# Kernel tuning notes

Measured on AMD Instinct MI355X. Metric: run time of the kernel, lower is better.

## Reference

```python
import jax, jax.numpy as jnp
import numpy as np

N_USERS = 100000
N_ITEMS = 50000
DIM = 64
NNZ = 10000000
N_LAYERS = 3
N_NODES = N_USERS + N_ITEMS


def setup_inputs() -> dict:
    key = jax.random.key(0)
    k1, k2, k3, k4, k5 = jax.random.split(key, 5)
    # xavier-ish init for embedding tables
    user_emb = jax.random.normal(k1, (N_USERS, DIM), dtype=jnp.float32) * 0.1
    item_emb = jax.random.normal(k2, (N_ITEMS, DIM), dtype=jnp.float32) * 0.1
    # COO representation of the symmetric normalized adjacency
    adj_row = jax.random.randint(k3, (NNZ,), 0, N_NODES, dtype=jnp.int32)
    adj_col = jax.random.randint(k4, (NNZ,), 0, N_NODES, dtype=jnp.int32)
    # normalized values are small positive numbers (d_i^-1/2 * d_j^-1/2)
    adj_val = jax.random.uniform(k5, (NNZ,), dtype=jnp.float32) * 0.01
    return {
        "user_emb": user_emb,
        "item_emb": item_emb,
        "adj_val": adj_val,
        "adj_row": adj_row,
        "adj_col": adj_col,
    }


def reference(user_emb, item_emb, adj_val, adj_row, adj_col):
    # all_emb: [N_NODES, DIM]
    all_emb = jnp.concatenate([user_emb, item_emb], axis=0)
    acc = all_emb  # running sum over layers (incl. layer 0)
    emb = all_emb
    for _ in range(N_LAYERS):
        # SpMM: out[r] += val * emb[c] for each edge (r, c)
        msgs = adj_val[:, None] * emb[adj_col]  # [NNZ, DIM]
        emb = jax.ops.segment_sum(msgs, adj_row, num_segments=N_NODES)
        acc = acc + emb
    mean_emb = acc / jnp.float32(N_LAYERS + 1)
    return mean_emb[:N_USERS], mean_emb[N_USERS:]
```

## Files before the change

### kernel.cpp

```cpp
#include <hip/hip_runtime.h>

#define N_USERS 100000
#define N_ITEMS 50000
#define N_NODES (N_USERS + N_ITEMS)
#define DIM 64
#define NNZ_TOTAL 10000000
#define TOTAL (N_NODES * DIM)
#define TOTAL4 (TOTAL / 4)
#define USZ4 (N_USERS * DIM / 4)

#define BROWS 256
#define NB ((N_NODES + BROWS - 1) / BROWS)
#define SCHUNK 8192
#define SGRD ((NNZ_TOTAL + SCHUNK - 1) / SCHUNK)
#define COLMASK 0x3FFFFu

#define CTSH 14
#define NT 10
#define NKEY (BROWS * NT)

__device__ __forceinline__ float bf2f(unsigned short u) {
    return __uint_as_float(((unsigned)u) << 16);
}
__device__ __forceinline__ unsigned short f2bf(float f) {
    unsigned b = __float_as_uint(f);
    b += 0x7FFFu + ((b >> 16) & 1u);
    return (unsigned short)(b >> 16);
}

__global__ __launch_bounds__(256) void k_init(const float4* __restrict__ user,
                                              const float4* __restrict__ item,
                                              ushort4* __restrict__ T0,
                                              float4* __restrict__ acc) {
    const int stride = gridDim.x * blockDim.x;
    for (int i = blockIdx.x * blockDim.x + threadIdx.x; i < TOTAL4; i += stride) {
        float4 v = (i < USZ4) ? user[i] : item[i - USZ4];
        acc[i] = v;
        ushort4 t;
        t.x = f2bf(v.x); t.y = f2bf(v.y); t.z = f2bf(v.z); t.w = f2bf(v.w);
        T0[i] = t;
    }
}

__global__ __launch_bounds__(256) void k_lhist(const int* __restrict__ row,
                                               int* __restrict__ cnt) {
    __shared__ int h[NB];
    for (int i = threadIdx.x; i < NB; i += 256) h[i] = 0;
    __syncthreads();
    const int g = blockIdx.x;
    const int lo = g * SCHUNK;
    const int hi = (lo + SCHUNK < NNZ_TOTAL) ? lo + SCHUNK : NNZ_TOTAL;
    for (int e = lo + threadIdx.x; e < hi; e += 256)
        atomicAdd(&h[row[e] >> 8], 1);
    __syncthreads();
    for (int b = threadIdx.x; b < NB; b += 256)
        cnt[b * SGRD + g] = h[b];
}

__global__ __launch_bounds__(256) void k_rowsum(const int* __restrict__ cnt,
                                                int* __restrict__ rowsum) {
    __shared__ int lds[256];
    const int b = blockIdx.x;
    const int t = threadIdx.x;
    int s = 0;
    for (int k = t; k < SGRD; k += 256) s += cnt[b * SGRD + k];
    lds[t] = s;
    __syncthreads();
    #pragma unroll
    for (int off = 128; off > 0; off >>= 1) {
        if (t < off) lds[t] += lds[t + off];
        __syncthreads();
    }
    if (t == 0) rowsum[b] = lds[0];
}

__global__ __launch_bounds__(1024) void k_sscan(const int* __restrict__ rowsum,
                                                int* __restrict__ bbase) {
    __shared__ int lds[1024];
    const int t = threadIdx.x;
    const int x = (t < NB) ? rowsum[t] : 0;
    lds[t] = x;
    __syncthreads();
    for (int off = 1; off < 1024; off <<= 1) {
        const int y = (t >= off) ? lds[t - off] : 0;
        __syncthreads();
        lds[t] += y;
        __syncthreads();
    }
    if (t < NB) bbase[t] = lds[t] - x;
    if (t == 1023) bbase[NB] = lds[1023];
}

__global__ __launch_bounds__(1024) void k_rowscan(int* __restrict__ cnt,
                                                  const int* __restrict__ bbase) {
    __shared__ int lds[1024];
    const int b = blockIdx.x;
    const int t = threadIdx.x;
    const int i0 = 2 * t, i1 = 2 * t + 1;
    const int a0 = (i0 < SGRD) ? cnt[b * SGRD + i0] : 0;
    const int a1 = (i1 < SGRD) ? cnt[b * SGRD + i1] : 0;
    const int s = a0 + a1;
    lds[t] = s;
    __syncthreads();
    for (int off = 1; off < 1024; off <<= 1) {
        const int y = (t >= off) ? lds[t - off] : 0;
        __syncthreads();
        lds[t] += y;
        __syncthreads();
    }
    const int pre = bbase[b] + lds[t] - s;
    if (i0 < SGRD) cnt[b * SGRD + i0] = pre;
    if (i1 < SGRD) cnt[b * SGRD + i1] = pre + a0;
}

__global__ __launch_bounds__(1024) void k_lscatter(const int* __restrict__ row,
                                                   const int* __restrict__ col,
                                                   const float* __restrict__ val,
                                                   const int* __restrict__ cnt,
                                                   const int* __restrict__ bbase,
                                                   uint2* __restrict__ tmp) {
    __shared__ uint2 stage[SCHUNK];
    __shared__ int lstartp[1024];
    __shared__ int gbase[NB];
    __shared__ int cur[NB];
    __shared__ int scratch[1024];

    const int g = blockIdx.x;
    const int t = threadIdx.x;
    const int lo = g * SCHUNK;
    const int hi = (lo + SCHUNK < NNZ_TOTAL) ? lo + SCHUNK : NNZ_TOTAL;
    const int n = hi - lo;

    int lcnt = 0;
    if (t < NB) {
        const int base = cnt[t * SGRD + g];
        gbase[t] = base;
        const int nxt = (g == SGRD - 1) ? bbase[t + 1] : cnt[t * SGRD + g + 1];
        lcnt = nxt - base;
    }
    scratch[t] = lcnt;
    __syncthreads();

    for (int off = 1; off < 1024; off <<= 1) {
        const int y = (t >= off) ? scratch[t - off] : 0;
        __syncthreads();
        scratch[t] += y;
        __syncthreads();
    }
    const int ls = (t < NB) ? scratch[t] - lcnt : n;
    lstartp[t] = ls;
    if (t < NB) cur[t] = ls;
    __syncthreads();

    for (int e = lo + t; e < hi; e += 1024) {
        const int r = row[e];
        const unsigned meta = ((unsigned)(r & (BROWS - 1)) << 18) | (unsigned)col[e];
        const int p = atomicAdd(&cur[r >> 8], 1);
        stage[p] = make_uint2(meta, __float_as_uint(val[e]));
    }
    __syncthreads();

    for (int l = t; l < n; l += 1024) {
        int blo = 0, bhi = 1024;
        #pragma unroll
        for (int s = 0; s < 10; ++s) {
            const int mid = (blo + bhi) >> 1;
            if (lstartp[mid] <= l) blo = mid; else bhi = mid;
        }
        tmp[gbase[blo] + (l - lstartp[blo])] = stage[l];
    }
}

__global__ __launch_bounds__(256) void k_bsort(const uint2* __restrict__ tmp,
                                               uint2* __restrict__ csr,
                                               const int* __restrict__ bbase,
                                               int* __restrict__ row_offs) {
    __shared__ int cnt[NKEY];
    __shared__ int curl[NKEY];
    __shared__ int part[256];
    const int tid = threadIdx.x;
    const int b = blockIdx.x;
    const int s = bbase[b];
    const int e = bbase[b + 1];

    for (int k = tid; k < NKEY; k += 256) cnt[k] = 0;
    __syncthreads();
    for (int j = s + tid; j < e; j += 256) {
        const unsigned m = tmp[j].x;
        const int key = (int)(m >> 18) * NT + (int)((m & COLMASK) >> CTSH);
        atomicAdd(&cnt[key], 1);
    }
    __syncthreads();
    const int lo = tid * NT;
    int ssum = 0;
    #pragma unroll
    for (int k = 0; k < NT; ++k) ssum += cnt[lo + k];
    part[tid] = ssum;
    __syncthreads();
    for (int off = 1; off < 256; off <<= 1) {
        const int y = (tid >= off) ? part[tid - off] : 0;
        __syncthreads();
        part[tid] += y;
        __syncthreads();
    }
    int base = part[tid] - ssum;
    #pragma unroll
    for (int k = 0; k < NT; ++k) {
        const int c = cnt[lo + k];
        cnt[lo + k] = base;
        curl[lo + k] = base;
        base += c;
    }
    __syncthreads();
    {
        const int gr = b * BROWS + tid;
        if (gr < N_NODES) row_offs[gr] = s + cnt[tid * NT];
    }
    for (int j = s + tid; j < e; j += 256) {
        const uint2 u = tmp[j];
        const unsigned m = u.x;
        const int key = (int)(m >> 18) * NT + (int)((m & COLMASK) >> CTSH);
        const int p = atomicAdd(&curl[key], 1);
        csr[s + p] = u;
    }
    if (b == 0 && tid == 0) row_offs[N_NODES] = NNZ_TOTAL;
}

template <bool FINAL>
__global__ __launch_bounds__(256) void k_spmm_bf16(const ushort4* __restrict__ T4,
                                                   ushort4* __restrict__ U4,
                                                   float4* __restrict__ ACC4,
                                                   const int* __restrict__ offs,
                                                   const uint2* __restrict__ csr) {
    const int lane = threadIdx.x & 63;
    const int sub  = lane >> 4;
    const int d4   = lane & 15;
    const int r = blockIdx.x * 4 + (threadIdx.x >> 6);
    const int s = offs[r];
    const int e = offs[r + 1];
    float4 acc = make_float4(0.f, 0.f, 0.f, 0.f);
    int j = s + sub;
    for (; j + 12 < e; j += 16) {
        const uint2 e0 = csr[j];
        const uint2 e1 = csr[j + 4];
        const uint2 e2 = csr[j + 8];
        const uint2 e3 = csr[j + 12];
        const ushort4 g0 = T4[(size_t)(e0.x & COLMASK) * 16 + d4];
        const ushort4 g1 = T4[(size_t)(e1.x & COLMASK) * 16 + d4];
        const ushort4 g2 = T4[(size_t)(e2.x & COLMASK) * 16 + d4];
        const ushort4 g3 = T4[(size_t)(e3.x & COLMASK) * 16 + d4];
        const float v0 = __uint_as_float(e0.y);
        const float v1 = __uint_as_float(e1.y);
        const float v2 = __uint_as_float(e2.y);
        const float v3 = __uint_as_float(e3.y);
        acc.x += v0 * bf2f(g0.x) + v1 * bf2f(g1.x) + v2 * bf2f(g2.x) + v3 * bf2f(g3.x);
        acc.y += v0 * bf2f(g0.y) + v1 * bf2f(g1.y) + v2 * bf2f(g2.y) + v3 * bf2f(g3.y);
        acc.z += v0 * bf2f(g0.z) + v1 * bf2f(g1.z) + v2 * bf2f(g2.z) + v3 * bf2f(g3.z);
        acc.w += v0 * bf2f(g0.w) + v1 * bf2f(g1.w) + v2 * bf2f(g2.w) + v3 * bf2f(g3.w);
    }
    for (; j + 4 < e; j += 8) {
        const uint2 e0 = csr[j];
        const uint2 e1 = csr[j + 4];
        const ushort4 g0 = T4[(size_t)(e0.x & COLMASK) * 16 + d4];
        const ushort4 g1 = T4[(size_t)(e1.x & COLMASK) * 16 + d4];
        const float v0 = __uint_as_float(e0.y);
        const float v1 = __uint_as_float(e1.y);
        acc.x += v0 * bf2f(g0.x) + v1 * bf2f(g1.x);
        acc.y += v0 * bf2f(g0.y) + v1 * bf2f(g1.y);
        acc.z += v0 * bf2f(g0.z) + v1 * bf2f(g1.z);
        acc.w += v0 * bf2f(g0.w) + v1 * bf2f(g1.w);
    }
    if (j < e) {
        const uint2 e0 = csr[j];
        const ushort4 g0 = T4[(size_t)(e0.x & COLMASK) * 16 + d4];
        const float v0 = __uint_as_float(e0.y);
        acc.x += v0 * bf2f(g0.x);
        acc.y += v0 * bf2f(g0.y);
        acc.z += v0 * bf2f(g0.z);
        acc.w += v0 * bf2f(g0.w);
    }
    #pragma unroll
    for (int m = 16; m <= 32; m <<= 1) {
        acc.x += __shfl_xor(acc.x, m, 64);
        acc.y += __shfl_xor(acc.y, m, 64);
        acc.z += __shfl_xor(acc.z, m, 64);
        acc.w += __shfl_xor(acc.w, m, 64);
    }
    if (sub == 0) {
        const size_t idx = (size_t)r * 16 + d4;
        float4 a = ACC4[idx];
        if (FINAL) {
            a.x = (a.x + acc.x) * 0.25f;
            a.y = (a.y + acc.y) * 0.25f;
            a.z = (a.z + acc.z) * 0.25f;
            a.w = (a.w + acc.w) * 0.25f;
            ACC4[idx] = a;
        } else {
            ushort4 t;
            t.x = f2bf(acc.x); t.y = f2bf(acc.y); t.z = f2bf(acc.z); t.w = f2bf(acc.w);
            U4[idx] = t;
            a.x += acc.x;
            a.y += acc.y;
            a.z += acc.z;
            a.w += acc.w;
            ACC4[idx] = a;
        }
    }
}

__global__ __launch_bounds__(256) void k_init_f32(const float4* __restrict__ user,
                                                  const float4* __restrict__ item,
                                                  float4* __restrict__ A,
                                                  float4* __restrict__ acc) {
    const int stride = gridDim.x * blockDim.x;
    for (int i = blockIdx.x * blockDim.x + threadIdx.x; i < TOTAL4; i += stride) {
        float4 v = (i < USZ4) ? user[i] : item[i - USZ4];
        A[i] = v;
        acc[i] = v;
    }
}

__global__ __launch_bounds__(256) void k_spmm_atomic(const float* __restrict__ A,
                                                     float* __restrict__ B,
                                                     const float* __restrict__ val,
                                                     const int* __restrict__ row,
                                                     const int* __restrict__ col) {
    const int lane = threadIdx.x & 63;
    int wave = blockIdx.x * (blockDim.x >> 6) + (threadIdx.x >> 6);
    const int nw = gridDim.x * (blockDim.x >> 6);
    for (int e = wave; e < NNZ_TOTAL; e += nw) {
        const float x = A[col[e] * DIM + lane];
        unsafeAtomicAdd(&B[row[e] * DIM + lane], val[e] * x);
    }
}

__global__ __launch_bounds__(256) void k_accadd(float4* __restrict__ acc,
                                                const float4* __restrict__ B) {
    const int stride = gridDim.x * blockDim.x;
    for (int i = blockIdx.x * blockDim.x + threadIdx.x; i < TOTAL4; i += stride) {
        float4 a = acc[i];
        const float4 b = B[i];
        a.x += b.x; a.y += b.y; a.z += b.z; a.w += b.w;
        acc[i] = a;
    }
}

__global__ __launch_bounds__(256) void k_final(float4* __restrict__ acc,
                                               const float4* __restrict__ B) {
    const int stride = gridDim.x * blockDim.x;
    for (int i = blockIdx.x * blockDim.x + threadIdx.x; i < TOTAL4; i += stride) {
        float4 a = acc[i];
        const float4 b = B[i];
        a.x = (a.x + b.x) * 0.25f;
        a.y = (a.y + b.y) * 0.25f;
        a.z = (a.z + b.z) * 0.25f;
        a.w = (a.w + b.w) * 0.25f;
        acc[i] = a;
    }
}

extern "C" void kernel_launch(void* const* d_in, const int* in_sizes, int n_in,
                              void* d_out, int out_size, void* d_ws, size_t ws_size,
                              hipStream_t stream) {
    const float* user = (const float*)d_in[0];
    const float* item = (const float*)d_in[1];
    const float* val  = (const float*)d_in[2];
    const int*   row  = (const int*)d_in[3];
    const int*   col  = (const int*)d_in[4];

    float* acc = (float*)d_out;
    const int eltBlocks = 2048;

    const size_t CSR_BYTES = (size_t)NNZ_TOTAL * 8;
    uint2* csr  = (uint2*)d_ws;
    int*   cnt  = (int*)d_ws;
    char*  reg1 = (char*)d_ws + CSR_BYTES;
    uint2* tmp  = (uint2*)reg1;
    ushort4* T0 = (ushort4*)reg1;
    ushort4* T1 = T0 + TOTAL4;
    int* row_offs = (int*)(reg1 + CSR_BYTES);
    int* bbase    = row_offs + N_NODES + 1;
    int* rowsum   = bbase + NB + 1;

    const size_t needed =
        2 * CSR_BYTES + (size_t)(N_NODES + 1 + 2 * NB + 2) * 4;

    if (ws_size >= needed) {
        k_lhist<<<SGRD, 256, 0, stream>>>(row, cnt);
        k_rowsum<<<NB, 256, 0, stream>>>(cnt, rowsum);
        k_sscan<<<1, 1024, 0, stream>>>(rowsum, bbase);
        k_rowscan<<<NB, 1024, 0, stream>>>(cnt, bbase);
        k_lscatter<<<SGRD, 1024, 0, stream>>>(row, col, val, cnt, bbase, tmp);
        k_bsort<<<NB, 256, 0, stream>>>(tmp, csr, bbase, row_offs);

        k_init<<<eltBlocks, 256, 0, stream>>>((const float4*)user, (const float4*)item,
                                              T0, (float4*)acc);

        const int rowBlocks = N_NODES / 4;
        k_spmm_bf16<false><<<rowBlocks, 256, 0, stream>>>(
            T0, T1, (float4*)acc, row_offs, csr);
        k_spmm_bf16<false><<<rowBlocks, 256, 0, stream>>>(
            T1, T0, (float4*)acc, row_offs, csr);
        k_spmm_bf16<true><<<rowBlocks, 256, 0, stream>>>(
            T0, T1, (float4*)acc, row_offs, csr);
        return;
    }

    float* A2 = (float*)d_ws;
    float* B2 = A2 + TOTAL;
    k_init_f32<<<eltBlocks, 256, 0, stream>>>((const float4*)user, (const float4*)item,
                                              (float4*)A2, (float4*)acc);
    float* Af = A2;
    float* Bf = B2;
    for (int layer = 0; layer < 3; ++layer) {
        hipMemsetAsync(Bf, 0, (size_t)TOTAL * sizeof(float), stream);
        k_spmm_atomic<<<2048, 256, 0, stream>>>(Af, Bf, val, row, col);
        if (layer < 2) {
            k_accadd<<<eltBlocks, 256, 0, stream>>>((float4*)acc, (const float4*)Bf);
            float* t = Af; Af = Bf; Bf = t;
        } else {
            k_final<<<eltBlocks, 256, 0, stream>>>((float4*)acc, (const float4*)Bf);
        }
    }
}
```

Measured before the change: 787.8 us.

## Tile SpMM gathers by column range with LDS row accumulators

The per-bucket sort now orders edges by column tile first, then by row. A new kernel builds per-(tile,row) offset tables. The SpMM kernel assigns 74 rows to each block and walks the 10 column tiles in sequence, accumulating partial row sums in shared memory, so that gathers from the bf16 embedding table stay within a roughly 2 MB column window that can stay cache-resident. In exchange it adds a preprocessing kernel, a block barrier after every tile, and very short per-(row,tile) segments. The old 4-way unrolled gather loop becomes a single-gather loop, which lowers memory-level parallelism.

```diff
diff --git a/kernel.cpp b/kernel.cpp
--- a/kernel.cpp
+++ b/kernel.cpp
@@ -18,6 +18,10 @@
 #define CTSH 14
 #define NT 10
 #define NKEY (BROWS * NT)
+
+#define ROWS_PB 74
+#define RPW 19
+#define SPMM_GRID ((N_NODES + ROWS_PB - 1) / ROWS_PB)
 
 __device__ __forceinline__ float bf2f(unsigned short u) {
     return __uint_as_float(((unsigned)u) << 16);
@@ -173,8 +177,7 @@
 
 __global__ __launch_bounds__(256) void k_bsort(const uint2* __restrict__ tmp,
                                                uint2* __restrict__ csr,
-                                               const int* __restrict__ bbase,
-                                               int* __restrict__ row_offs) {
+                                               const int* __restrict__ bbase) {
     __shared__ int cnt[NKEY];
     __shared__ int curl[NKEY];
     __shared__ int part[256];
@@ -187,7 +190,7 @@
     __syncthreads();
     for (int j = s + tid; j < e; j += 256) {
         const unsigned m = tmp[j].x;
-        const int key = (int)(m >> 18) * NT + (int)((m & COLMASK) >> CTSH);
+        const int key = (int)((m & COLMASK) >> CTSH) * BROWS + (int)(m >> 18);
         atomicAdd(&cnt[key], 1);
     }
     __syncthreads();
@@ -207,103 +210,131 @@
     #pragma unroll
     for (int k = 0; k < NT; ++k) {
         const int c = cnt[lo + k];
-        cnt[lo + k] = base;
         curl[lo + k] = base;
         base += c;
     }
     __syncthreads();
-    {
-        const int gr = b * BROWS + tid;
-        if (gr < N_NODES) row_offs[gr] = s + cnt[tid * NT];
-    }
     for (int j = s + tid; j < e; j += 256) {
         const uint2 u = tmp[j];
         const unsigned m = u.x;
-        const int key = (int)(m >> 18) * NT + (int)((m & COLMASK) >> CTSH);
+        const int key = (int)((m & COLMASK) >> CTSH) * BROWS + (int)(m >> 18);
         const int p = atomicAdd(&curl[key], 1);
         csr[s + p] = u;
     }
-    if (b == 0 && tid == 0) row_offs[N_NODES] = NNZ_TOTAL;
+}
+
+__global__ __launch_bounds__(256) void k_rtoffs(const uint2* __restrict__ csr,
+                                                const int* __restrict__ bbase,
+                                                int* __restrict__ rt_abs) {
+    __shared__ int cnt[NKEY];
+    __shared__ int part[256];
+    const int tid = threadIdx.x;
+    const int b = blockIdx.x;
+    const int s = bbase[b];
+    const int e = bbase[b + 1];
+    for (int k = tid; k < NKEY; k += 256) cnt[k] = 0;
+    __syncthreads();
+    for (int j = s + tid; j < e; j += 256) {
+        const unsigned m = csr[j].x;
+        const int key = (int)((m & COLMASK) >> CTSH) * BROWS + (int)(m >> 18);
+        atomicAdd(&cnt[key], 1);
+    }
+    __syncthreads();
+    const int lo = tid * NT;
+    int ssum = 0;
+    #pragma unroll
+    for (int k = 0; k < NT; ++k) ssum += cnt[lo + k];
+    part[tid] = ssum;
+    __syncthreads();
+    for (int off = 1; off < 256; off <<= 1) {
+        const int y = (tid >= off) ? part[tid - off] : 0;
+        __syncthreads();
+        part[tid] += y;
+        __syncthreads();
+    }
+    int base = part[tid] - ssum;
+    #pragma unroll
+    for (int k = 0; k < NT; ++k) {
+        rt_abs[(size_t)b * NKEY + lo + k] = s + base;
+        base += cnt[lo + k];
+    }
+    if (b == 0 && tid == 0) rt_abs[(size_t)NB * NKEY] = NNZ_TOTAL;
 }
 
 template <bool FINAL>
-__global__ __launch_bounds__(256) void k_spmm_bf16(const ushort4* __restrict__ T4,
-                                                   ushort4* __restrict__ U4,
-                                                   float4* __restrict__ ACC4,
-                                                   const int* __restrict__ offs,
-                                                   const uint2* __restrict__ csr) {
-    const int lane = threadIdx.x & 63;
+__global__ __launch_bounds__(256, 8) void k_spmm_tile(const ushort4* __restrict__ T4,
+                                                      ushort4* __restrict__ U4,
+                                                      float4* __restrict__ ACC4,
+                                                      const int* __restrict__ rt_abs,
+                                                      const uint2* __restrict__ csr) {
+    __shared__ float4 accL[ROWS_PB * 16];
+    const int tid  = threadIdx.x;
+    const int lane = tid & 63;
     const int sub  = lane >> 4;
     const int d4   = lane & 15;
-    const int r = blockIdx.x * 4 + (threadIdx.x >> 6);
-    const int s = offs[r];
-    const int e = offs[r + 1];
-    float4 acc = make_float4(0.f, 0.f, 0.f, 0.f);
-    int j = s + sub;
-    for (; j + 12 < e; j += 16) {
-        const uint2 e0 = csr[j];
-        const uint2 e1 = csr[j + 4];
-        const uint2 e2 = csr[j + 8];
-        const uint2 e3 = csr[j + 12];
-        const ushort4 g0 = T4[(size_t)(e0.x & COLMASK) * 16 + d4];
-        const ushort4 g1 = T4[(size_t)(e1.x & COLMASK) * 16 + d4];
-        const ushort4 g2 = T4[(size_t)(e2.x & COLMASK) * 16 + d4];
-        const ushort4 g3 = T4[(size_t)(e3.x & COLMASK) * 16 + d4];
-        const float v0 = __uint_as_float(e0.y);
-        const float v1 = __uint_as_float(e1.y);
-        const float v2 = __uint_as_float(e2.y);
-        const float v3 = __uint_as_float(e3.y);
-        acc.x += v0 * bf2f(g0.x) + v1 * bf2f(g1.x) + v2 * bf2f(g2.x) + v3 * bf2f(g3.x);
-        acc.y += v0 * bf2f(g0.y) + v1 * bf2f(g1.y) + v2 * bf2f(g2.y) + v3 * bf2f(g3.y);
-        acc.z += v0 * bf2f(g0.z) + v1 * bf2f(g1.z) + v2 * bf2f(g2.z) + v3 * bf2f(g3.z);
-        acc.w += v0 * bf2f(g0.w) + v1 * bf2f(g1.w) + v2 * bf2f(g2.w) + v3 * bf2f(g3.w);
-    }
-    for (; j + 4 < e; j += 8) {
-        const uint2 e0 = csr[j];
-        const uint2 e1 = csr[j + 4];
-        const ushort4 g0 = T4[(size_t)(e0.x & COLMASK) * 16 + d4];
-        const ushort4 g1 = T4[(size_t)(e1.x & COLMASK) * 16 + d4];
-        const float v0 = __uint_as_float(e0.y);
-        const float v1 = __uint_as_float(e1.y);
-        acc.x += v0 * bf2f(g0.x) + v1 * bf2f(g1.x);
-        acc.y += v0 * bf2f(g0.y) + v1 * bf2f(g1.y);
-        acc.z += v0 * bf2f(g0.z) + v1 * bf2f(g1.z);
-        acc.w += v0 * bf2f(g0.w) + v1 * bf2f(g1.w);
-    }
-    if (j < e) {
-        const uint2 e0 = csr[j];
-        const ushort4 g0 = T4[(size_t)(e0.x & COLMASK) * 16 + d4];
-        const float v0 = __uint_as_float(e0.y);
-        acc.x += v0 * bf2f(g0.x);
-        acc.y += v0 * bf2f(g0.y);
-        acc.z += v0 * bf2f(g0.z);
-        acc.w += v0 * bf2f(g0.w);
-    }
-    #pragma unroll
-    for (int m = 16; m <= 32; m <<= 1) {
-        acc.x += __shfl_xor(acc.x, m, 64);
-        acc.y += __shfl_xor(acc.y, m, 64);
-        acc.z += __shfl_xor(acc.z, m, 64);
-        acc.w += __shfl_xor(acc.w, m, 64);
-    }
-    if (sub == 0) {
-        const size_t idx = (size_t)r * 16 + d4;
-        float4 a = ACC4[idx];
+    const int w    = tid >> 6;
+    const int rbase = blockIdx.x * ROWS_PB;
+
+    for (int i = tid; i < ROWS_PB * 16; i += 256)
+        accL[i] = make_float4(0.f, 0.f, 0.f, 0.f);
+    __syncthreads();
+
+    const int r0 = w * RPW;
+    const int r1 = (r0 + RPW < ROWS_PB) ? r0 + RPW : ROWS_PB;
+
+    for (int t = 0; t < NT; ++t) {
+        for (int r = r0; r < r1; ++r) {
+            const int gr = rbase + r;
+            if (gr >= N_NODES) break;
+            const int B  = gr >> 8;
+            const int lr = gr & (BROWS - 1);
+            const size_t ix = (size_t)B * NKEY + t * BROWS + lr;
+            const int s = rt_abs[ix];
+            const int e = rt_abs[ix + 1];
+            float4 a = make_float4(0.f, 0.f, 0.f, 0.f);
+            for (int j = s + sub; j < e; j += 4) {
+                const uint2 u = csr[j];
+                const ushort4 g = T4[(size_t)(u.x & COLMASK) * 16 + d4];
+                const float v = __uint_as_float(u.y);
+                a.x += v * bf2f(g.x);
+                a.y += v * bf2f(g.y);
+                a.z += v * bf2f(g.z);
+                a.w += v * bf2f(g.w);
+            }
+            #pragma unroll
+            for (int m = 16; m <= 32; m <<= 1) {
+                a.x += __shfl_xor(a.x, m, 64);
+                a.y += __shfl_xor(a.y, m, 64);
+                a.z += __shfl_xor(a.z, m, 64);
+                a.w += __shfl_xor(a.w, m, 64);
+            }
+            if (sub == 0) {
+                float4 c = accL[r * 16 + d4];
+                c.x += a.x; c.y += a.y; c.z += a.z; c.w += a.w;
+                accL[r * 16 + d4] = c;
+            }
+        }
+        __syncthreads();
+    }
+
+    for (int i = tid; i < ROWS_PB * 16; i += 256) {
+        const int gr = rbase + (i >> 4);
+        if (gr >= N_NODES) break;
+        const size_t gi = (size_t)gr * 16 + (i & 15);
+        float4 a = ACC4[gi];
+        const float4 c = accL[i];
         if (FINAL) {
-            a.x = (a.x + acc.x) * 0.25f;
-            a.y = (a.y + acc.y) * 0.25f;
-            a.z = (a.z + acc.z) * 0.25f;
-            a.w = (a.w + acc.w) * 0.25f;
-            ACC4[idx] = a;
+            a.x = (a.x + c.x) * 0.25f;
+            a.y = (a.y + c.y) * 0.25f;
+            a.z = (a.z + c.z) * 0.25f;
+            a.w = (a.w + c.w) * 0.25f;
+            ACC4[gi] = a;
         } else {
-            ushort4 t;
-            t.x = f2bf(acc.x); t.y = f2bf(acc.y); t.z = f2bf(acc.z); t.w = f2bf(acc.w);
-            U4[idx] = t;
-            a.x += acc.x;
-            a.y += acc.y;
-            a.z += acc.z;
-            a.w += acc.w;
-            ACC4[idx] = a;
+            ushort4 tt;
+            tt.x = f2bf(c.x); tt.y = f2bf(c.y); tt.z = f2bf(c.z); tt.w = f2bf(c.w);
+            U4[gi] = tt;
+            a.x += c.x; a.y += c.y; a.z += c.z; a.w += c.w;
+            ACC4[gi] = a;
         }
     }
 }
@@ -378,12 +409,11 @@
     uint2* tmp  = (uint2*)reg1;
     ushort4* T0 = (ushort4*)reg1;
     ushort4* T1 = T0 + TOTAL4;
-    int* row_offs = (int*)(reg1 + CSR_BYTES);
-    int* bbase    = row_offs + N_NODES + 1;
-    int* rowsum   = bbase + NB + 1;
-
-    const size_t needed =
-        2 * CSR_BYTES + (size_t)(N_NODES + 1 + 2 * NB + 2) * 4;
+    int* rt_abs = (int*)(T1 + TOTAL4);
+    int* bbase  = (int*)(reg1 + CSR_BYTES);
+    int* rowsum = bbase + NB + 1;
+
+    const size_t needed = 2 * CSR_BYTES + (size_t)(2 * NB + 1) * 4;
 
     if (ws_size >= needed) {
         k_lhist<<<SGRD, 256, 0, stream>>>(row, cnt);
@@ -391,18 +421,18 @@
         k_sscan<<<1, 1024, 0, stream>>>(rowsum, bbase);
         k_rowscan<<<NB, 1024, 0, stream>>>(cnt, bbase);
         k_lscatter<<<SGRD, 1024, 0, stream>>>(row, col, val, cnt, bbase, tmp);
-        k_bsort<<<NB, 256, 0, stream>>>(tmp, csr, bbase, row_offs);
+        k_bsort<<<NB, 256, 0, stream>>>(tmp, csr, bbase);
+        k_rtoffs<<<NB, 256, 0, stream>>>(csr, bbase, rt_abs);
 
         k_init<<<eltBlocks, 256, 0, stream>>>((const float4*)user, (const float4*)item,
                                               T0, (float4*)acc);
 
-        const int rowBlocks = N_NODES / 4;
-        k_spmm_bf16<false><<<rowBlocks, 256, 0, stream>>>(
-            T0, T1, (float4*)acc, row_offs, csr);
-        k_spmm_bf16<false><<<rowBlocks, 256, 0, stream>>>(
-            T1, T0, (float4*)acc, row_offs, csr);
-        k_spmm_bf16<true><<<rowBlocks, 256, 0, stream>>>(
-            T0, T1, (float4*)acc, row_offs, csr);
+        k_spmm_tile<false><<<SPMM_GRID, 256, 0, stream>>>(
+            T0, T1, (float4*)acc, rt_abs, csr);
+        k_spmm_tile<false><<<SPMM_GRID, 256, 0, stream>>>(
+            T1, T0, (float4*)acc, rt_abs, csr);
+        k_spmm_tile<true><<<SPMM_GRID, 256, 0, stream>>>(
+            T0, T1, (float4*)acc, rt_abs, csr);
         return;
     }
 
```

After: 1.324 ms. +68.1%, slower.
